# Performance work log

Measured on AMD Instinct MI355X. Metric: run time of the kernel, lower is better.

## Reference

```python
import jax, jax.numpy as jnp
import numpy as np

B, S, D = 4, 2048, 768
H = 12
HD = D // H  # 64

def setup_inputs() -> dict:
    key = jax.random.key(0)
    ks = jax.random.split(key, 5)
    scale = 0.02
    return {
        "x": jax.random.normal(ks[0], (B, S, D), dtype=jnp.float32),
        "w_qkv": jax.random.normal(ks[1], (D, 3 * D), dtype=jnp.float32) * scale,
        "b_qkv": jax.random.normal(ks[2], (3 * D,), dtype=jnp.float32) * scale,
        "w_proj": jax.random.normal(ks[3], (D, D), dtype=jnp.float32) * scale,
        "b_proj": jax.random.normal(ks[4], (D,), dtype=jnp.float32) * scale,
    }

def reference(x, w_qkv, b_qkv, w_proj, b_proj):
    bsz, seq_len, dim = x.shape
    qkv = x @ w_qkv + b_qkv                      # [B,S,3D]
    q, k, v = jnp.split(qkv, 3, axis=-1)
    # [B,S,D] -> [B,H,S,HD]
    def heads(t):
        return t.reshape(bsz, seq_len, H, HD).transpose(0, 2, 1, 3)
    q, k, v = heads(q), heads(k), heads(v)
    scores = jnp.einsum('bhqd,bhkd->bhqk', q, k) * (1.0 / np.sqrt(HD))
    causal = jnp.tril(jnp.ones((seq_len, seq_len), dtype=bool))
    scores = jnp.where(causal[None, None], scores, -jnp.inf)
    attn = jax.nn.softmax(scores.astype(jnp.float32), axis=-1).astype(scores.dtype)
    y = jnp.einsum('bhqk,bhkd->bhqd', attn, v)   # [B,H,S,HD]
    y = y.transpose(0, 2, 1, 3).reshape(bsz, seq_len, dim)
    return y @ w_proj + b_proj
```

## Files before the change

### kernel.cpp

```cpp
#include <hip/hip_runtime.h>
#include <hip/hip_bf16.h>
#include <cstdint>

#define BDIM 768
#define HN 12
#define HDIM 64
#define SEQ 2048
#define BATCH 4
#define MTOT (BATCH * SEQ)

typedef __attribute__((ext_vector_type(8))) short bfrag;
typedef __attribute__((ext_vector_type(4))) float f32x4;

union pfu { bfrag f; unsigned u[4]; };

static __device__ __forceinline__ unsigned short f2bf(float f) {
    union { float f; unsigned u; } v; v.f = f;
    unsigned r = v.u + 0x7FFF + ((v.u >> 16) & 1);
    return (unsigned short)(r >> 16);
}

static __device__ __forceinline__ float fexp2(float x) {
    float r; asm("v_exp_f32 %0, %1" : "=v"(r) : "v"(x)); return r;
}

static __device__ __forceinline__ unsigned cvt_pk_bf16(float lo, float hi) {
    unsigned r;
    asm("v_cvt_pk_bf16_f32 %0, %1, %2" : "=v"(r) : "v"(lo), "v"(hi));
    return r;
}

#if __has_builtin(__builtin_amdgcn_permlane32_swap) && __has_builtin(__builtin_amdgcn_permlane16_swap)
#define HAVE_PERMLANE 1
#else
#define HAVE_PERMLANE 0
#endif

static __device__ __forceinline__ float redmax16(float x) {
#if HAVE_PERMLANE
    union { float f; unsigned u; } a; a.f = x;
    auto r = __builtin_amdgcn_permlane16_swap(a.u, a.u, false, false);
    union { unsigned u; float f; } p, q; p.u = r[0]; q.u = r[1];
    return fmaxf(p.f, q.f);
#else
    return fmaxf(x, __shfl_xor(x, 16));
#endif
}

static __device__ __forceinline__ float redmax32(float x) {
#if HAVE_PERMLANE
    union { float f; unsigned u; } a; a.f = x;
    auto r = __builtin_amdgcn_permlane32_swap(a.u, a.u, false, false);
    union { unsigned u; float f; } p, q; p.u = r[0]; q.u = r[1];
    return fmaxf(p.f, q.f);
#else
    return fmaxf(x, __shfl_xor(x, 32));
#endif
}

__global__ __launch_bounds__(256) void conv_f32_bf16(
    const float* __restrict__ in, unsigned short* __restrict__ out, int n8,
    int* __restrict__ qctr)
{
    if (blockIdx.x == 0 && threadIdx.x < 8) qctr[threadIdx.x] = 0;
    const int i = blockIdx.x * 256 + threadIdx.x;
    if (i >= n8) return;
    const float4 a = ((const float4*)in)[i * 2];
    const float4 b = ((const float4*)in)[i * 2 + 1];
    bfrag o;
    o[0] = f2bf(a.x); o[1] = f2bf(a.y); o[2] = f2bf(a.z); o[3] = f2bf(a.w);
    o[4] = f2bf(b.x); o[5] = f2bf(b.y); o[6] = f2bf(b.z); o[7] = f2bf(b.w);
    ((bfrag*)out)[i] = o;
}

__global__ __launch_bounds__(256) void transpose_f32_bf16(
    const float* __restrict__ in, unsigned short* __restrict__ out, int R, int C)
{
    __shared__ unsigned short t[64][72];
    const int tid = threadIdx.x;
    const int c0 = blockIdx.x * 64, r0 = blockIdx.y * 64;
    #pragma unroll
    for (int i = 0; i < 4; ++i) {
        const int r = (tid >> 4) + i * 16;
        const int c = (tid & 15) * 4;
        const float4 v = *(const float4*)&in[(size_t)(r0 + r) * C + c0 + c];
        t[c + 0][r] = f2bf(v.x);
        t[c + 1][r] = f2bf(v.y);
        t[c + 2][r] = f2bf(v.z);
        t[c + 3][r] = f2bf(v.w);
    }
    __syncthreads();
    #pragma unroll
    for (int i = 0; i < 2; ++i) {
        const int c = (tid >> 3) + i * 32;
        const int r = (tid & 7) * 8;
        *(bfrag*)&out[(size_t)(c0 + c) * R + r0 + r] = *(const bfrag*)&t[c][r];
    }
}

__global__ __launch_bounds__(256) void gemm_qkv(
    const unsigned short* __restrict__ A,
    const unsigned short* __restrict__ Bt,
    const float* __restrict__ bias,
    unsigned short* __restrict__ qb,
    unsigned short* __restrict__ kb,
    unsigned short* __restrict__ vTt)
{
    __shared__ unsigned short As[128 * 64];
    __shared__ unsigned short Bs[128 * 64];

    const int tid  = threadIdx.x;
    const int lane = tid & 63;
    const int wid  = tid >> 6;
    const int l15  = lane & 15;
    const int l4   = lane >> 4;
    const int m0 = blockIdx.y * 128;
    const int n0 = blockIdx.x * 128;
    const int wm = (wid >> 1) * 64;
    const int wn = (wid & 1) * 64;

    f32x4 acc[4][4] = {};

    for (int k0 = 0; k0 < BDIM; k0 += 64) {
        __syncthreads();
        #pragma unroll
        for (int i = 0; i < 4; ++i) {
            const int row = wid * 32 + i * 8 + (lane >> 3);
            const int ck  = (((lane & 7) ^ (row & 7)) * 8);
            __builtin_amdgcn_global_load_lds(
                (const __attribute__((address_space(1))) void*)(A + (size_t)(m0 + row) * BDIM + k0 + ck),
                (__attribute__((address_space(3))) void*)(As + (wid * 4 + i) * 512),
                16, 0, 0);
            __builtin_amdgcn_global_load_lds(
                (const __attribute__((address_space(1))) void*)(Bt + (size_t)(n0 + row) * BDIM + k0 + ck),
                (__attribute__((address_space(3))) void*)(Bs + (wid * 4 + i) * 512),
                16, 0, 0);
        }
        __syncthreads();

        #pragma unroll
        for (int ks = 0; ks < 2; ++ks) {
            bfrag af[4], bfv[4];
            #pragma unroll
            for (int mi = 0; mi < 4; ++mi) {
                const int row = wm + mi * 16 + l15;
                const int ch  = (ks * 4 + l4) ^ (row & 7);
                af[mi] = *(const bfrag*)(As + row * 64 + ch * 8);
            }
            #pragma unroll
            for (int ni = 0; ni < 4; ++ni) {
                const int row = wn + ni * 16 + l15;
                const int ch  = (ks * 4 + l4) ^ (row & 7);
                bfv[ni] = *(const bfrag*)(Bs + row * 64 + ch * 8);
            }
            #pragma unroll
            for (int mi = 0; mi < 4; ++mi)
                #pragma unroll
                for (int ni = 0; ni < 4; ++ni)
                    acc[mi][ni] = __builtin_amdgcn_mfma_f32_16x16x32_bf16(
                        af[mi], bfv[ni], acc[mi][ni], 0, 0, 0);
        }
    }

    const int nb = n0 + wn;
    if (nb < 1536) {
        unsigned short* dst = (nb < 768) ? qb : kb;
        const int coff = (nb < 768) ? 0 : 768;
        #pragma unroll
        for (int mi = 0; mi < 4; ++mi)
            #pragma unroll
            for (int ni = 0; ni < 4; ++ni) {
                const int n = nb + ni * 16 + l15;
                const float bv = bias[n];
                #pragma unroll
                for (int r = 0; r < 4; ++r) {
                    const int m = m0 + wm + mi * 16 + l4 * 4 + r;
                    dst[(size_t)m * BDIM + (n - coff)] = f2bf(acc[mi][ni][r] + bv);
                }
            }
    } else {
        #pragma unroll
        for (int mi = 0; mi < 4; ++mi)
            #pragma unroll
            for (int ni = 0; ni < 4; ++ni) {
                const int n = nb + ni * 16 + l15;
                const float bv = bias[n];
                const size_t vrow = (size_t)(m0 >> 11) * 768 + (n - 1536);
                const int mbase = m0 + wm + mi * 16 + l4 * 4;
                const int scol = mbase & (SEQ - 1);
                uint2 u2;
                u2.x = (unsigned)f2bf(acc[mi][ni][0] + bv)
                     | ((unsigned)f2bf(acc[mi][ni][1] + bv) << 16);
                u2.y = (unsigned)f2bf(acc[mi][ni][2] + bv)
                     | ((unsigned)f2bf(acc[mi][ni][3] + bv) << 16);
                *(uint2*)(vTt + vrow * SEQ + scol) = u2;
            }
    }
}

__global__ __launch_bounds__(256) void gemm_proj(
    const unsigned short* __restrict__ A,
    const unsigned short* __restrict__ Bt,
    const float* __restrict__ bias,
    float* __restrict__ C)
{
    __shared__ unsigned short As[64 * 64];
    __shared__ unsigned short Bs[128 * 64];

    const int tid  = threadIdx.x;
    const int lane = tid & 63;
    const int wid  = tid >> 6;
    const int l15  = lane & 15;
    const int l4   = lane >> 4;
    const int m0 = blockIdx.y * 64;
    const int n0 = blockIdx.x * 128;
    const int wm = (wid >> 1) * 32;
    const int wn = (wid & 1) * 64;

    f32x4 acc[2][4] = {};

    for (int k0 = 0; k0 < BDIM; k0 += 64) {
        __syncthreads();
        #pragma unroll
        for (int i = 0; i < 2; ++i) {
            const int row = wid * 16 + i * 8 + (lane >> 3);
            const int ck  = (((lane & 7) ^ (row & 7)) * 8);
            __builtin_amdgcn_global_load_lds(
                (const __attribute__((address_space(1))) void*)(A + (size_t)(m0 + row) * BDIM + k0 + ck),
                (__attribute__((address_space(3))) void*)(As + (wid * 16 + i * 8) * 64),
                16, 0, 0);
        }
        #pragma unroll
        for (int i = 0; i < 4; ++i) {
            const int row = wid * 32 + i * 8 + (lane >> 3);
            const int ck  = (((lane & 7) ^ (row & 7)) * 8);
            __builtin_amdgcn_global_load_lds(
                (const __attribute__((address_space(1))) void*)(Bt + (size_t)(n0 + row) * BDIM + k0 + ck),
                (__attribute__((address_space(3))) void*)(Bs + (wid * 32 + i * 8) * 64),
                16, 0, 0);
        }
        __syncthreads();

        #pragma unroll
        for (int ks = 0; ks < 2; ++ks) {
            bfrag af[2], bfv[4];
            #pragma unroll
            for (int mi = 0; mi < 2; ++mi) {
                const int row = wm + mi * 16 + l15;
                const int ch  = (ks * 4 + l4) ^ (row & 7);
                af[mi] = *(const bfrag*)(As + row * 64 + ch * 8);
            }
            #pragma unroll
            for (int ni = 0; ni < 4; ++ni) {
                const int row = wn + ni * 16 + l15;
                const int ch  = (ks * 4 + l4) ^ (row & 7);
                bfv[ni] = *(const bfrag*)(Bs + row * 64 + ch * 8);
            }
            #pragma unroll
            for (int mi = 0; mi < 2; ++mi)
                #pragma unroll
                for (int ni = 0; ni < 4; ++ni)
                    acc[mi][ni] = __builtin_amdgcn_mfma_f32_16x16x32_bf16(
                        af[mi], bfv[ni], acc[mi][ni], 0, 0, 0);
        }
    }

    #pragma unroll
    for (int mi = 0; mi < 2; ++mi)
        #pragma unroll
        for (int ni = 0; ni < 4; ++ni) {
            const int n = n0 + wn + ni * 16 + l15;
            const float bv = bias[n];
            #pragma unroll
            for (int r = 0; r < 4; ++r) {
                const int m = m0 + wm + mi * 16 + l4 * 4 + r;
                C[(size_t)m * BDIM + n] = acc[mi][ni][r] + bv;
            }
        }
}

#define C2 0.18033688011112042f
#define THR 8.0f

__global__ __launch_bounds__(256, 2) void attn_flash_mfma(
    const unsigned short* __restrict__ qb,
    const unsigned short* __restrict__ kb,
    const unsigned short* __restrict__ vT,
    unsigned short* __restrict__ yatt,
    int* __restrict__ qctr)
{
    __shared__ unsigned short Ks[2][64 * 64];
    __shared__ unsigned short Vs[2][64 * 64];

    const int hint = blockIdx.x & 7;
    const int tid  = threadIdx.x;
    const int lane = tid & 63;
    const int wid  = tid >> 6;
    const int l15  = lane & 15;
    const int l4   = lane >> 4;

    bfrag onesf;
    #pragma unroll
    for (int j = 0; j < 8; ++j) onesf[j] = (short)0x3F80;

    for (;;) {
        __syncthreads();
        if (tid == 0) *(int*)&Ks[0][0] = atomicAdd(&qctr[hint], 1);
        __syncthreads();
        const int it = *(const int*)&Ks[0][0];
        if (it >= 96) break;
        __syncthreads();

        const int bh = hint * 6 + (it % 6);
        const int p  = 15 - (it / 6);
        const int h = bh % HN, b = bh / HN;
        const int q0 = p * 128;
        const int ktmax = 2 * p + 1;

        const unsigned short* kg = kb + (size_t)b * SEQ * BDIM + h * HDIM;
        const unsigned short* vg = vT + (size_t)bh * HDIM * SEQ;

        bfrag qf[2][2];
        {
            const unsigned short* qr0 =
                qb + (size_t)(b * SEQ + q0 + wid * 16 + l15) * BDIM + h * HDIM;
            qf[0][0] = *(const bfrag*)(qr0 + l4 * 8);
            qf[0][1] = *(const bfrag*)(qr0 + 32 + l4 * 8);
            const unsigned short* qr1 = qr0 + (size_t)64 * BDIM;
            qf[1][0] = *(const bfrag*)(qr1 + l4 * 8);
            qf[1][1] = *(const bfrag*)(qr1 + 32 + l4 * 8);
        }

        f32x4 acc0[4] = {}, acc1[4] = {};
        f32x4 accl0 = {}, accl1 = {};
        float m0v = -3.0e38f, m1v = -3.0e38f;

        pfu pf0[2], pf1[2];
        bfrag vr[2][4];
        #pragma unroll
        for (int ks = 0; ks < 2; ++ks) {
            #pragma unroll
            for (int i = 0; i < 4; ++i) { pf0[ks].u[i] = 0u; pf1[ks].u[i] = 0u; }
            #pragma unroll
            for (int ds = 0; ds < 4; ++ds)
                #pragma unroll
                for (int j = 0; j < 8; ++j) vr[ks][ds][j] = 0;
        }

        auto stage = [&](int bufi, int ktile) {
            const int k0 = ktile * 64;
            #pragma unroll
            for (int i = 0; i < 2; ++i) {
                const int row = wid * 16 + i * 8 + (lane >> 3);
                const int ck  = ((lane & 7) ^ (row & 7)) * 8;
                __builtin_amdgcn_global_load_lds(
                    (const __attribute__((address_space(1))) void*)(kg + (size_t)(k0 + row) * BDIM + ck),
                    (__attribute__((address_space(3))) void*)(&Ks[bufi][(wid * 16 + i * 8) * 64]),
                    16, 0, 0);
                __builtin_amdgcn_global_load_lds(
                    (const __attribute__((address_space(1))) void*)(vg + (size_t)row * SEQ + k0 + ck),
                    (__attribute__((address_space(3))) void*)(&Vs[bufi][(wid * 16 + i * 8) * 64]),
                    16, 0, 0);
            }
        };

        auto softmax_dance = [&](f32x4* s, float& mm, pfu* pf, f32x4* acc, f32x4& accl) {
            float mx = s[0][0];
            #pragma unroll
            for (int cs = 0; cs < 4; ++cs)
                #pragma unroll
                for (int r = 0; r < 4; ++r) mx = fmaxf(mx, s[cs][r]);
            mx = redmax16(mx);
            mx = redmax32(mx);
            const float mx2 = mx * C2;

            if (!__all(mx2 <= mm + THR)) {
                const float mnew = fmaxf(mm, mx2);
                const float fac  = fexp2(mm - mnew);
                mm = mnew;
                #pragma unroll
                for (int r = 0; r < 4; ++r) {
                    const float fr = __shfl(fac, (lane & 48) | (l4 * 4 + r));
                    #pragma unroll
                    for (int ds = 0; ds < 4; ++ds) acc[ds][r] *= fr;
                    accl[r] *= fr;
                }
            }

            #pragma unroll
            for (int cs = 0; cs < 4; ++cs)
                #pragma unroll
                for (int r = 0; r < 4; ++r)
                    s[cs][r] = fexp2(fmaf(s[cs][r], C2, -mm));

            unsigned pk[4][2];
            #pragma unroll
            for (int cs = 0; cs < 4; ++cs) {
                pk[cs][0] = cvt_pk_bf16(s[cs][0], s[cs][1]);
                pk[cs][1] = cvt_pk_bf16(s[cs][2], s[cs][3]);
            }
            #pragma unroll
            for (int ks = 0; ks < 2; ++ks)
                #pragma unroll
                for (int i = 0; i < 2; ++i) {
#if HAVE_PERMLANE
                    auto r1 = __builtin_amdgcn_permlane32_swap(
                        pk[ks * 2][i], pk[ks * 2 + 1][i], false, false);
                    auto r2 = __builtin_amdgcn_permlane16_swap(r1[0], r1[1], false, false);
                    pf[ks].u[i]     = r2[0];
                    pf[ks].u[2 + i] = r2[1];
#else
                    const unsigned A  = pk[ks * 2][i];
                    const unsigned B  = pk[ks * 2 + 1][i];
                    const unsigned Ax = __shfl_xor(A, 32);
                    const unsigned Bx = __shfl_xor(B, 32);
                    const unsigned P1 = (l4 < 2) ? A : Bx;
                    const unsigned P2 = (l4 < 2) ? Ax : B;
                    const unsigned S1 = __shfl_xor(P1, 16);
                    const unsigned S2 = __shfl_xor(P2, 16);
                    pf[ks].u[i]     = (l4 & 1) ? S2 : P1;
                    pf[ks].u[2 + i] = (l4 & 1) ? P2 : S1;
#endif
                }
        };

        stage(0, 0);
        __syncthreads();

        int buf = 0;
        for (int kt = 0;;) {
            if (kt < ktmax) stage(buf ^ 1, kt + 1);

            const unsigned short* Kb = Ks[buf];
            const unsigned short* Vb = Vs[buf];

            f32x4 s0[4] = {}, s1[4] = {};
            __builtin_amdgcn_s_setprio(1);
            #pragma unroll
            for (int ks = 0; ks < 2; ++ks) {
                #pragma unroll
                for (int cs = 0; cs < 4; ++cs) {
                    const int row = cs * 16 + l15;
                    const int ch  = (ks * 4 + l4) ^ (row & 7);
                    const bfrag kf = *(const bfrag*)(Kb + row * 64 + ch * 8);
                    s0[cs] = __builtin_amdgcn_mfma_f32_16x16x32_bf16(kf, qf[0][ks], s0[cs], 0, 0, 0);
                    s1[cs] = __builtin_amdgcn_mfma_f32_16x16x32_bf16(kf, qf[1][ks], s1[cs], 0, 0, 0);
                }
            }
            #pragma unroll
            for (int ks = 0; ks < 2; ++ks) {
                #pragma unroll
                for (int ds = 0; ds < 4; ++ds) {
                    acc0[ds] = __builtin_amdgcn_mfma_f32_16x16x32_bf16(pf0[ks].f, vr[ks][ds], acc0[ds], 0, 0, 0);
                    acc1[ds] = __builtin_amdgcn_mfma_f32_16x16x32_bf16(pf1[ks].f, vr[ks][ds], acc1[ds], 0, 0, 0);
                }
                accl0 = __builtin_amdgcn_mfma_f32_16x16x32_bf16(pf0[ks].f, onesf, accl0, 0, 0, 0);
                accl1 = __builtin_amdgcn_mfma_f32_16x16x32_bf16(pf1[ks].f, onesf, accl1, 0, 0, 0);
            }
            __builtin_amdgcn_s_setprio(0);

            #pragma unroll
            for (int ks = 0; ks < 2; ++ks)
                #pragma unroll
                for (int ds = 0; ds < 4; ++ds) {
                    const int vrow = ds * 16 + l15;
                    const int vch  = (ks * 4 + l4) ^ (vrow & 7);
                    vr[ks][ds] = *(const bfrag*)(Vb + vrow * 64 + vch * 8);
                }

            if (kt >= 2 * p) {
                const int qg = q0 + wid * 16 + l15;
                #pragma unroll
                for (int cs = 0; cs < 4; ++cs)
                    #pragma unroll
                    for (int r = 0; r < 4; ++r) {
                        const int kgl = kt * 64 + cs * 16 + l4 * 4 + r;
                        if (kgl > qg)      s0[cs][r] = -3.0e38f;
                        if (kgl > qg + 64) s1[cs][r] = -3.0e38f;
                    }
            }

            softmax_dance(s0, m0v, pf0, acc0, accl0);
            softmax_dance(s1, m1v, pf1, acc1, accl1);

            if (kt == ktmax) break;
            __syncthreads();
            buf ^= 1; ++kt;
        }

        #pragma unroll
        for (int ks = 0; ks < 2; ++ks) {
            #pragma unroll
            for (int ds = 0; ds < 4; ++ds) {
                acc0[ds] = __builtin_amdgcn_mfma_f32_16x16x32_bf16(pf0[ks].f, vr[ks][ds], acc0[ds], 0, 0, 0);
                acc1[ds] = __builtin_amdgcn_mfma_f32_16x16x32_bf16(pf1[ks].f, vr[ks][ds], acc1[ds], 0, 0, 0);
            }
            accl0 = __builtin_amdgcn_mfma_f32_16x16x32_bf16(pf0[ks].f, onesf, accl0, 0, 0, 0);
            accl1 = __builtin_amdgcn_mfma_f32_16x16x32_bf16(pf1[ks].f, onesf, accl1, 0, 0, 0);
        }

        #pragma unroll
        for (int r = 0; r < 4; ++r) {
            const float iv0 = 1.f / accl0[r];
            const float iv1 = 1.f / accl1[r];
            unsigned short* o0 =
                yatt + (size_t)(b * SEQ + q0 + wid * 16 + l4 * 4 + r) * BDIM + h * HDIM;
            unsigned short* o1 = o0 + (size_t)64 * BDIM;
            #pragma unroll
            for (int ds = 0; ds < 4; ++ds) {
                o0[ds * 16 + l15] = f2bf(acc0[ds][r] * iv0);
                o1[ds * 16 + l15] = f2bf(acc1[ds][r] * iv1);
            }
        }
    }
}

extern "C" void kernel_launch(void* const* d_in, const int* in_sizes, int n_in,
                              void* d_out, int out_size, void* d_ws, size_t ws_size,
                              hipStream_t stream)
{
    const float* x      = (const float*)d_in[0];
    const float* w_qkv  = (const float*)d_in[1];
    const float* b_qkv  = (const float*)d_in[2];
    const float* w_proj = (const float*)d_in[3];
    const float* b_proj = (const float*)d_in[4];
    float* out = (float*)d_out;

    unsigned short* xb   = (unsigned short*)d_ws;
    unsigned short* qb   = xb  + (size_t)MTOT * BDIM;
    unsigned short* kbuf = qb  + (size_t)MTOT * BDIM;
    unsigned short* vT   = kbuf + (size_t)MTOT * BDIM;
    unsigned short* yatt = vT  + (size_t)MTOT * BDIM;
    unsigned short* wqT  = yatt + (size_t)MTOT * BDIM;
    unsigned short* wpT  = wqT + (size_t)3 * BDIM * BDIM;
    int*            qctr = (int*)(wpT + (size_t)BDIM * BDIM);

    conv_f32_bf16<<<(MTOT * BDIM / 8 + 255) / 256, 256, 0, stream>>>(
        x, xb, MTOT * BDIM / 8, qctr);
    transpose_f32_bf16<<<dim3(3 * BDIM / 64, BDIM / 64), 256, 0, stream>>>(
        w_qkv, wqT, BDIM, 3 * BDIM);
    transpose_f32_bf16<<<dim3(BDIM / 64, BDIM / 64), 256, 0, stream>>>(
        w_proj, wpT, BDIM, BDIM);

    gemm_qkv<<<dim3(3 * BDIM / 128, MTOT / 128), 256, 0, stream>>>(
        xb, wqT, b_qkv, qb, kbuf, vT);

    attn_flash_mfma<<<dim3(1024), 256, 0, stream>>>(qb, kbuf, vT, yatt, qctr);

    gemm_proj<<<dim3(BDIM / 128, MTOT / 64), 256, 0, stream>>>(
        yatt, wpT, b_proj, out);
}
```

Baseline: 141.6 us.

## Triple-buffer attention K/V staging, swizzle GEMM workgroup order, halve attention grid

```diff
diff --git a/kernel.cpp b/kernel.cpp
--- a/kernel.cpp
+++ b/kernel.cpp
@@ -114,8 +114,13 @@
     const int wid  = tid >> 6;
     const int l15  = lane & 15;
     const int l4   = lane >> 4;
-    const int m0 = blockIdx.y * 128;
-    const int n0 = blockIdx.x * 128;
+
+    const int nwg  = (int)(gridDim.x * gridDim.y);
+    const int flat = (int)(blockIdx.y * gridDim.x + blockIdx.x);
+    const int swz  = (flat & 7) * (nwg >> 3) + (flat >> 3);
+    const int m0 = (swz / (int)gridDim.x) * 128;
+    const int n0 = (swz % (int)gridDim.x) * 128;
+
     const int wm = (wid >> 1) * 64;
     const int wn = (wid & 1) * 64;
 
@@ -212,8 +217,13 @@
     const int wid  = tid >> 6;
     const int l15  = lane & 15;
     const int l4   = lane >> 4;
-    const int m0 = blockIdx.y * 64;
-    const int n0 = blockIdx.x * 128;
+
+    const int nwg  = (int)(gridDim.x * gridDim.y);
+    const int flat = (int)(blockIdx.y * gridDim.x + blockIdx.x);
+    const int swz  = (flat & 7) * (nwg >> 3) + (flat >> 3);
+    const int m0 = (swz / (int)gridDim.x) * 64;
+    const int n0 = (swz % (int)gridDim.x) * 128;
+
     const int wm = (wid >> 1) * 32;
     const int wn = (wid & 1) * 64;
 
@@ -289,8 +299,8 @@
     unsigned short* __restrict__ yatt,
     int* __restrict__ qctr)
 {
-    __shared__ unsigned short Ks[2][64 * 64];
-    __shared__ unsigned short Vs[2][64 * 64];
+    __shared__ unsigned short Ks[3][64 * 64];
+    __shared__ unsigned short Vs[3][64 * 64];
 
     const int hint = blockIdx.x & 7;
     const int tid  = threadIdx.x;
@@ -425,14 +435,17 @@
         };
 
         stage(0, 0);
-        __syncthreads();
-
-        int buf = 0;
-        for (int kt = 0;;) {
-            if (kt < ktmax) stage(buf ^ 1, kt + 1);
-
-            const unsigned short* Kb = Ks[buf];
-            const unsigned short* Vb = Vs[buf];
+        stage(1, 1);
+        asm volatile("s_waitcnt vmcnt(4) lgkmcnt(0)\ns_barrier" ::: "memory");
+
+        int kt = 0;
+        for (;;) {
+            const int cb = kt % 3;
+            const bool willstage = (kt + 2 <= ktmax);
+            if (willstage) stage((kt + 2) % 3, kt + 2);
+
+            const unsigned short* Kb = Ks[cb];
+            const unsigned short* Vb = Vs[cb];
 
             f32x4 s0[4] = {}, s1[4] = {};
             __builtin_amdgcn_s_setprio(1);
@@ -484,8 +497,12 @@
             softmax_dance(s1, m1v, pf1, acc1, accl1);
 
             if (kt == ktmax) break;
-            __syncthreads();
-            buf ^= 1; ++kt;
+            if (willstage) {
+                asm volatile("s_waitcnt vmcnt(4) lgkmcnt(0)\ns_barrier" ::: "memory");
+            } else {
+                asm volatile("s_waitcnt vmcnt(0) lgkmcnt(0)\ns_barrier" ::: "memory");
+            }
+            ++kt;
         }
 
         #pragma unroll
@@ -545,7 +562,7 @@
     gemm_qkv<<<dim3(3 * BDIM / 128, MTOT / 128), 256, 0, stream>>>(
         xb, wqT, b_qkv, qb, kbuf, vT);
 
-    attn_flash_mfma<<<dim3(1024), 256, 0, stream>>>(qb, kbuf, vT, yatt, qctr);
+    attn_flash_mfma<<<dim3(512), 256, 0, stream>>>(qb, kbuf, vT, yatt, qctr);
 
     gemm_proj<<<dim3(BDIM / 128, MTOT / 64), 256, 0, stream>>>(
         yatt, wpT, b_proj, out);
```

Measured after the change: 137.6 us. 1.03x faster.

## Load V directly into registers, swizzle GEMM block order, shrink attention grid

Applied to the files above, without the earlier changes.

```diff
diff --git a/kernel.cpp b/kernel.cpp
--- a/kernel.cpp
+++ b/kernel.cpp
@@ -114,8 +114,13 @@
     const int wid  = tid >> 6;
     const int l15  = lane & 15;
     const int l4   = lane >> 4;
-    const int m0 = blockIdx.y * 128;
-    const int n0 = blockIdx.x * 128;
+
+    const int nwg  = (int)(gridDim.x * gridDim.y);
+    const int flat = (int)(blockIdx.y * gridDim.x + blockIdx.x);
+    const int swz  = (flat & 7) * (nwg >> 3) + (flat >> 3);
+    const int m0 = (swz / (int)gridDim.x) * 128;
+    const int n0 = (swz % (int)gridDim.x) * 128;
+
     const int wm = (wid >> 1) * 64;
     const int wn = (wid & 1) * 64;
 
@@ -212,8 +217,13 @@
     const int wid  = tid >> 6;
     const int l15  = lane & 15;
     const int l4   = lane >> 4;
-    const int m0 = blockIdx.y * 64;
-    const int n0 = blockIdx.x * 128;
+
+    const int nwg  = (int)(gridDim.x * gridDim.y);
+    const int flat = (int)(blockIdx.y * gridDim.x + blockIdx.x);
+    const int swz  = (flat & 7) * (nwg >> 3) + (flat >> 3);
+    const int m0 = (swz / (int)gridDim.x) * 64;
+    const int n0 = (swz % (int)gridDim.x) * 128;
+
     const int wm = (wid >> 1) * 32;
     const int wn = (wid & 1) * 64;
 
@@ -290,7 +300,6 @@
     int* __restrict__ qctr)
 {
     __shared__ unsigned short Ks[2][64 * 64];
-    __shared__ unsigned short Vs[2][64 * 64];
 
     const int hint = blockIdx.x & 7;
     const int tid  = threadIdx.x;
@@ -336,7 +345,7 @@
         float m0v = -3.0e38f, m1v = -3.0e38f;
 
         pfu pf0[2], pf1[2];
-        bfrag vr[2][4];
+        bfrag vrA[2][4], vrB[2][4];
         #pragma unroll
         for (int ks = 0; ks < 2; ++ks) {
             #pragma unroll
@@ -344,10 +353,10 @@
             #pragma unroll
             for (int ds = 0; ds < 4; ++ds)
                 #pragma unroll
-                for (int j = 0; j < 8; ++j) vr[ks][ds][j] = 0;
-        }
-
-        auto stage = [&](int bufi, int ktile) {
+                for (int j = 0; j < 8; ++j) vrA[ks][ds][j] = 0;
+        }
+
+        auto stageK = [&](int bufi, int ktile) {
             const int k0 = ktile * 64;
             #pragma unroll
             for (int i = 0; i < 2; ++i) {
@@ -357,11 +366,17 @@
                     (const __attribute__((address_space(1))) void*)(kg + (size_t)(k0 + row) * BDIM + ck),
                     (__attribute__((address_space(3))) void*)(&Ks[bufi][(wid * 16 + i * 8) * 64]),
                     16, 0, 0);
-                __builtin_amdgcn_global_load_lds(
-                    (const __attribute__((address_space(1))) void*)(vg + (size_t)row * SEQ + k0 + ck),
-                    (__attribute__((address_space(3))) void*)(&Vs[bufi][(wid * 16 + i * 8) * 64]),
-                    16, 0, 0);
-            }
+            }
+        };
+
+        auto loadV = [&](bfrag (&dst)[2][4], int ktile) {
+            const int k0 = ktile * 64;
+            #pragma unroll
+            for (int ks = 0; ks < 2; ++ks)
+                #pragma unroll
+                for (int ds = 0; ds < 4; ++ds)
+                    dst[ks][ds] = *(const bfrag*)(
+                        vg + (size_t)(ds * 16 + l15) * SEQ + k0 + ks * 32 + l4 * 8);
         };
 
         auto softmax_dance = [&](f32x4* s, float& mm, pfu* pf, f32x4* acc, f32x4& accl) {
@@ -424,15 +439,11 @@
                 }
         };
 
-        stage(0, 0);
-        __syncthreads();
-
-        int buf = 0;
-        for (int kt = 0;;) {
-            if (kt < ktmax) stage(buf ^ 1, kt + 1);
+        auto step = [&](bfrag (&vuse)[2][4], bfrag (&vload)[2][4], int kt, int buf) {
+            loadV(vload, kt);
+            if (kt < ktmax) stageK(buf ^ 1, kt + 1);
 
             const unsigned short* Kb = Ks[buf];
-            const unsigned short* Vb = Vs[buf];
 
             f32x4 s0[4] = {}, s1[4] = {};
             __builtin_amdgcn_s_setprio(1);
@@ -451,22 +462,13 @@
             for (int ks = 0; ks < 2; ++ks) {
                 #pragma unroll
                 for (int ds = 0; ds < 4; ++ds) {
-                    acc0[ds] = __builtin_amdgcn_mfma_f32_16x16x32_bf16(pf0[ks].f, vr[ks][ds], acc0[ds], 0, 0, 0);
-                    acc1[ds] = __builtin_amdgcn_mfma_f32_16x16x32_bf16(pf1[ks].f, vr[ks][ds], acc1[ds], 0, 0, 0);
+                    acc0[ds] = __builtin_amdgcn_mfma_f32_16x16x32_bf16(pf0[ks].f, vuse[ks][ds], acc0[ds], 0, 0, 0);
+                    acc1[ds] = __builtin_amdgcn_mfma_f32_16x16x32_bf16(pf1[ks].f, vuse[ks][ds], acc1[ds], 0, 0, 0);
                 }
                 accl0 = __builtin_amdgcn_mfma_f32_16x16x32_bf16(pf0[ks].f, onesf, accl0, 0, 0, 0);
                 accl1 = __builtin_amdgcn_mfma_f32_16x16x32_bf16(pf1[ks].f, onesf, accl1, 0, 0, 0);
             }
             __builtin_amdgcn_s_setprio(0);
-
-            #pragma unroll
-            for (int ks = 0; ks < 2; ++ks)
-                #pragma unroll
-                for (int ds = 0; ds < 4; ++ds) {
-                    const int vrow = ds * 16 + l15;
-                    const int vch  = (ks * 4 + l4) ^ (vrow & 7);
-                    vr[ks][ds] = *(const bfrag*)(Vb + vrow * 64 + vch * 8);
-                }
 
             if (kt >= 2 * p) {
                 const int qg = q0 + wid * 16 + l15;
@@ -482,21 +484,34 @@
 
             softmax_dance(s0, m0v, pf0, acc0, accl0);
             softmax_dance(s1, m1v, pf1, acc1, accl1);
-
-            if (kt == ktmax) break;
+        };
+
+        auto finalPV = [&](bfrag (&vuse)[2][4]) {
+            #pragma unroll
+            for (int ks = 0; ks < 2; ++ks) {
+                #pragma unroll
+                for (int ds = 0; ds < 4; ++ds) {
+                    acc0[ds] = __builtin_amdgcn_mfma_f32_16x16x32_bf16(pf0[ks].f, vuse[ks][ds], acc0[ds], 0, 0, 0);
+                    acc1[ds] = __builtin_amdgcn_mfma_f32_16x16x32_bf16(pf1[ks].f, vuse[ks][ds], acc1[ds], 0, 0, 0);
+                }
+                accl0 = __builtin_amdgcn_mfma_f32_16x16x32_bf16(pf0[ks].f, onesf, accl0, 0, 0, 0);
+                accl1 = __builtin_amdgcn_mfma_f32_16x16x32_bf16(pf1[ks].f, onesf, accl1, 0, 0, 0);
+            }
+        };
+
+        stageK(0, 0);
+        __syncthreads();
+
+        int kt = 0, buf = 0;
+        for (;;) {
+            step(vrA, vrB, kt, buf);
+            if (kt == ktmax) { finalPV(vrB); break; }
             __syncthreads();
             buf ^= 1; ++kt;
-        }
-
-        #pragma unroll
-        for (int ks = 0; ks < 2; ++ks) {
-            #pragma unroll
-            for (int ds = 0; ds < 4; ++ds) {
-                acc0[ds] = __builtin_amdgcn_mfma_f32_16x16x32_bf16(pf0[ks].f, vr[ks][ds], acc0[ds], 0, 0, 0);
-                acc1[ds] = __builtin_amdgcn_mfma_f32_16x16x32_bf16(pf1[ks].f, vr[ks][ds], acc1[ds], 0, 0, 0);
-            }
-            accl0 = __builtin_amdgcn_mfma_f32_16x16x32_bf16(pf0[ks].f, onesf, accl0, 0, 0, 0);
-            accl1 = __builtin_amdgcn_mfma_f32_16x16x32_bf16(pf1[ks].f, onesf, accl1, 0, 0, 0);
+            step(vrB, vrA, kt, buf);
+            if (kt == ktmax) { finalPV(vrA); break; }
+            __syncthreads();
+            buf ^= 1; ++kt;
         }
 
         #pragma unroll
@@ -545,7 +560,7 @@
     gemm_qkv<<<dim3(3 * BDIM / 128, MTOT / 128), 256, 0, stream>>>(
         xb, wqT, b_qkv, qb, kbuf, vT);
 
-    attn_flash_mfma<<<dim3(1024), 256, 0, stream>>>(qb, kbuf, vT, yatt, qctr);
+    attn_flash_mfma<<<dim3(640), 256, 0, stream>>>(qb, kbuf, vT, yatt, qctr);
 
     gemm_proj<<<dim3(BDIM / 128, MTOT / 64), 256, 0, stream>>>(
         yatt, wpT, b_proj, out);
```

Measured after the change: 149.8 us. 5.8% more time.
